# Optimization experiments

Measured on AMD Instinct MI355X. Metric: run time of the kernel, lower is better.

The kernel has to match this reference:

```python
import jax, jax.numpy as jnp
import numpy as np

HEAD_SIZE = 64

def setup_inputs() -> dict:
    key = jax.random.key(0)
    kx, kq, kk, kv = jax.random.split(key, 4)
    n_embd = 1024
    x = jax.random.normal(kx, (4, 2048, n_embd), dtype=jnp.float32)
    s = 1.0 / np.sqrt(n_embd)
    Wq = jax.random.normal(kq, (HEAD_SIZE, n_embd), dtype=jnp.float32) * s
    Wk = jax.random.normal(kk, (HEAD_SIZE, n_embd), dtype=jnp.float32) * s
    Wv = jax.random.normal(kv, (HEAD_SIZE, n_embd), dtype=jnp.float32) * s
    return {"x": x, "Wq": Wq, "Wk": Wk, "Wv": Wv}

def reference(x, Wq, Wk, Wv):
    # x: [B, T, C]; W*: [head_size, C] (torch nn.Linear weight layout, y = x @ W.T)
    B, T, C = x.shape
    q = jnp.einsum('btc,hc->bth', x, Wq)  # [B, T, H]
    k = jnp.einsum('btc,hc->bth', x, Wk)
    v = jnp.einsum('btc,hc->bth', x, Wv)
    att = jnp.einsum('bqh,bkh->bqk', q, k) / jnp.sqrt(jnp.float32(HEAD_SIZE))
    causal = jnp.tril(jnp.ones((T, T), dtype=bool))  # [T, T]
    att = jnp.where(causal, att, -jnp.inf)
    att = jax.nn.softmax(att, axis=-1)
    out = jnp.einsum('bqk,bkh->bqh', att, v)  # [B, T, H]
    return out
```

## Files before the change

### kernel.cpp

```cpp
#include <hip/hip_runtime.h>
#include <hip/hip_bf16.h>

#define NB 4
#define TT 2048
#define CC 1024
#define HS 64
#define L2E 1.4426950408889634f

typedef __attribute__((ext_vector_type(8))) short short8;
typedef __attribute__((ext_vector_type(4))) short short4v;
typedef __attribute__((ext_vector_type(4))) float floatx4;
typedef __attribute__((ext_vector_type(2))) float floatx2;

__device__ __forceinline__ short f2bf(float f) {
  union { float f; unsigned u; } x; x.f = f;
  unsigned r = (x.u + 0x7fffu + ((x.u >> 16) & 1u)) >> 16;
  return (short)r;
}

__device__ __forceinline__ short8 pack_bf16x8(floatx4 a, floatx4 b) {
  union { __hip_bfloat162 h[4]; short8 s; } u;
  u.h[0] = __float22bfloat162_rn(make_float2(a[0], a[1]));
  u.h[1] = __float22bfloat162_rn(make_float2(a[2], a[3]));
  u.h[2] = __float22bfloat162_rn(make_float2(b[0], b[1]));
  u.h[3] = __float22bfloat162_rn(make_float2(b[2], b[3]));
  return u.s;
}

#define KC 64
#define WTS 72

__global__ __launch_bounds__(768) void qkv_proj(const float* __restrict__ x,
                                                const float* __restrict__ wq,
                                                const float* __restrict__ wk,
                                                const float* __restrict__ wv,
                                                short* __restrict__ qb,
                                                short* __restrict__ kbuf,
                                                short* __restrict__ vtb) {
  __shared__ __align__(16) short wt[2][192 * WTS];
  __shared__ __align__(16) short xs[2][32 * WTS];

  const int tid  = threadIdx.x;
  const int lane = tid & 63;
  const int w    = tid >> 6;
  const int col  = lane & 15;
  const int quad = lane >> 4;
  const int row32 = blockIdx.x * 32;
  const int rg = w / 6;
  const int cg = w % 6;
  const int mat   = cg >> 1;
  const int hbase = (cg & 1) * 32;

  const int o0 = tid >> 3,         kk0 = (tid & 7) * 8;
  const int o1 = (768 + tid) >> 3, kk1 = ((768 + tid) & 7) * 8;
  const float* wsrc0 = (o0 < 64 ? wq + (size_t)o0 * CC
                                : wk + (size_t)(o0 - 64) * CC) + kk0;
  const float* wsrc1 = (o1 < 128 ? wk + (size_t)(o1 - 64) * CC
                                 : wv + (size_t)(o1 - 128) * CC) + kk1;
  const int xr = tid >> 3, xk = (tid & 7) * 8;
  const float* xsrc = x + (size_t)(row32 + xr) * CC + xk;

  floatx4 wa0 = *(const floatx4*)(wsrc0);
  floatx4 wc0 = *(const floatx4*)(wsrc0 + 4);
  floatx4 wa1 = *(const floatx4*)(wsrc1);
  floatx4 wc1 = *(const floatx4*)(wsrc1 + 4);
  floatx4 xA[2], xC[2];
  if (tid < 256) {
    xA[0] = *(const floatx4*)(xsrc);       xC[0] = *(const floatx4*)(xsrc + 4);
    xA[1] = *(const floatx4*)(xsrc + KC);  xC[1] = *(const floatx4*)(xsrc + KC + 4);
  }

  *(short8*)(&wt[0][o0 * WTS + kk0]) = pack_bf16x8(wa0, wc0);
  *(short8*)(&wt[0][o1 * WTS + kk1]) = pack_bf16x8(wa1, wc1);
  if (tid < 256) *(short8*)(&xs[0][xr * WTS + xk]) = pack_bf16x8(xA[0], xC[0]);
  __syncthreads();

  floatx4 acc0 = (floatx4){0.f, 0.f, 0.f, 0.f};
  floatx4 acc1 = (floatx4){0.f, 0.f, 0.f, 0.f};
  const int arow  = (rg * 16 + col) * WTS + quad * 8;
  const int brow0 = (cg * 32 + col) * WTS + quad * 8;
  const int brow1 = (cg * 32 + 16 + col) * WTS + quad * 8;

#pragma unroll 2
  for (int ch = 0; ch < 16; ++ch) {
    const int cur = ch & 1;
    if (ch < 15) {
      const int k0 = (ch + 1) * KC;
      wa0 = *(const floatx4*)(wsrc0 + k0);
      wc0 = *(const floatx4*)(wsrc0 + k0 + 4);
      wa1 = *(const floatx4*)(wsrc1 + k0);
      wc1 = *(const floatx4*)(wsrc1 + k0 + 4);
    }
    if (ch < 14 && tid < 256) {
      const int k0 = (ch + 2) * KC;
      xA[cur] = *(const floatx4*)(xsrc + k0);
      xC[cur] = *(const floatx4*)(xsrc + k0 + 4);
    }
#pragma unroll
    for (int kb2 = 0; kb2 < 2; ++kb2) {
      short8 a  = *(const short8*)(&xs[cur][arow + kb2 * 32]);
      short8 b0 = *(const short8*)(&wt[cur][brow0 + kb2 * 32]);
      short8 b1 = *(const short8*)(&wt[cur][brow1 + kb2 * 32]);
      acc0 = __builtin_amdgcn_mfma_f32_16x16x32_bf16(a, b0, acc0, 0, 0, 0);
      acc1 = __builtin_amdgcn_mfma_f32_16x16x32_bf16(a, b1, acc1, 0, 0, 0);
    }
    if (ch < 15) {
      __syncthreads();
      const int nxt = cur ^ 1;
      *(short8*)(&wt[nxt][o0 * WTS + kk0]) = pack_bf16x8(wa0, wc0);
      *(short8*)(&wt[nxt][o1 * WTS + kk1]) = pack_bf16x8(wa1, wc1);
      if (tid < 256)
        *(short8*)(&xs[nxt][xr * WTS + xk]) = pack_bf16x8(xA[nxt & 1], xC[nxt & 1]);
      __syncthreads();
    }
  }

  const int h0 = hbase + col;
  const int h1 = hbase + 16 + col;
  if (mat == 2) {
    int b = row32 >> 11;
    int t = (row32 & (TT - 1)) + rg * 16 + quad * 4;
    short4v o;
    o[0] = f2bf(acc0[0]); o[1] = f2bf(acc0[1]); o[2] = f2bf(acc0[2]); o[3] = f2bf(acc0[3]);
    *(short4v*)(vtb + (size_t)(b * HS + h0) * TT + t) = o;
    o[0] = f2bf(acc1[0]); o[1] = f2bf(acc1[1]); o[2] = f2bf(acc1[2]); o[3] = f2bf(acc1[3]);
    *(short4v*)(vtb + (size_t)(b * HS + h1) * TT + t) = o;
  } else {
    short* dst = (mat == 0) ? qb : kbuf;
    float s = (mat == 0) ? 0.125f : 1.0f;
#pragma unroll
    for (int r = 0; r < 4; ++r) {
      size_t row = (size_t)(row32 + rg * 16 + quad * 4 + r);
      dst[row * HS + h0] = f2bf(acc0[r] * s);
      dst[row * HS + h1] = f2bf(acc1[r] * s);
    }
  }
}

#define PST 72

__global__ __launch_bounds__(512, 4) void attn(const short* __restrict__ qb,
                                               const short* __restrict__ kb,
                                               const short* __restrict__ vtb,
                                               float* __restrict__ out) {
  __shared__ __align__(16) short pt[8][2][16 * PST];
  __shared__ float cl[8][16];
  __shared__ __align__(16) float co[8][16][64];

  const int tid  = threadIdx.x;
  const int lane = tid & 63;
  const int w    = tid >> 6;
  const int col  = lane & 15;
  const int quad = lane >> 4;
  const int b  = blockIdx.x & 3;
  const int qt = 127 - (blockIdx.x >> 2);
  const int t0 = qt * 16;

  const short* qbase = qb + (size_t)(b * TT + t0) * HS;
  const short* kbase = kb + (size_t)b * TT * HS;
  const short* vbase = vtb + (size_t)b * HS * TT;

  short8 qf0 = *(const short8*)(qbase + col * HS + quad * 8);
  short8 qf1 = *(const short8*)(qbase + col * HS + 32 + quad * 8);

  floatx4 oacc[4];
#pragma unroll
  for (int i = 0; i < 4; ++i) oacc[i] = (floatx4){0.f, 0.f, 0.f, 0.f};
  float lsum[4] = {0.f, 0.f, 0.f, 0.f};

  const int Nc = (t0 + 16 + 63) >> 6;

  short8 knA[4], knB[4];
  if (w < Nc) {
    const short* kp = kbase + (size_t)(w * 64) * HS + quad * 8;
#pragma unroll
    for (int j = 0; j < 4; ++j) {
      knA[j] = *(const short8*)(kp + (size_t)(j * 16 + col) * HS);
      knB[j] = *(const short8*)(kp + (size_t)(j * 16 + col) * HS + 32);
    }
  }

  int parity = 0;
  for (int c = w; c < Nc; c += 8, parity ^= 1) {
    const int kb0 = c * 64;

    floatx4 st[4];
#pragma unroll
    for (int j = 0; j < 4; ++j) st[j] = (floatx4){0.f, 0.f, 0.f, 0.f};
#pragma unroll
    for (int j = 0; j < 4; ++j) {
      st[j] = __builtin_amdgcn_mfma_f32_16x16x32_bf16(qf0, knA[j], st[j], 0, 0, 0);
      st[j] = __builtin_amdgcn_mfma_f32_16x16x32_bf16(qf1, knB[j], st[j], 0, 0, 0);
    }

    short8 vfA[4], vfB[4];
#pragma unroll
    for (int ht = 0; ht < 4; ++ht) {
      const short* vp = vbase + (size_t)(ht * 16 + col) * TT + kb0 + quad * 8;
      vfA[ht] = *(const short8*)(vp);
      vfB[ht] = *(const short8*)(vp + 32);
    }

    if (c + 8 < Nc) {
      const short* kpn = kbase + (size_t)((c + 8) * 64) * HS + quad * 8;
#pragma unroll
      for (int j = 0; j < 4; ++j) {
        knA[j] = *(const short8*)(kpn + (size_t)(j * 16 + col) * HS);
        knB[j] = *(const short8*)(kpn + (size_t)(j * 16 + col) * HS + 32);
      }
    }

    const bool diag = (kb0 + 63 > t0);
    short* pw = &pt[w][parity][0];

#pragma unroll
    for (int j = 0; j < 4; ++j) {
      if (diag) {
        int kcol = kb0 + j * 16 + col;
#pragma unroll
        for (int r = 0; r < 4; ++r)
          if (kcol > t0 + quad * 4 + r) st[j][r] = -1e30f;
      }
      float p0 = exp2f(st[j][0] * L2E);
      float p1 = exp2f(st[j][1] * L2E);
      float p2 = exp2f(st[j][2] * L2E);
      float p3 = exp2f(st[j][3] * L2E);
      lsum[0] += p0; lsum[1] += p1; lsum[2] += p2; lsum[3] += p3;
      union { __hip_bfloat162 h; short s[2]; } uA, uB;
      uA.h = __float22bfloat162_rn(make_float2(p0, p1));
      uB.h = __float22bfloat162_rn(make_float2(p2, p3));
      pw[(quad * 4 + 0) * PST + j * 16 + col] = uA.s[0];
      pw[(quad * 4 + 1) * PST + j * 16 + col] = uA.s[1];
      pw[(quad * 4 + 2) * PST + j * 16 + col] = uB.s[0];
      pw[(quad * 4 + 3) * PST + j * 16 + col] = uB.s[1];
    }
    short8 af0 = *(const short8*)(pw + col * PST + quad * 8);
    short8 af1 = *(const short8*)(pw + col * PST + 32 + quad * 8);

#pragma unroll
    for (int ht = 0; ht < 4; ++ht) {
      oacc[ht] = __builtin_amdgcn_mfma_f32_16x16x32_bf16(af0, vfA[ht], oacc[ht], 0, 0, 0);
      oacc[ht] = __builtin_amdgcn_mfma_f32_16x16x32_bf16(af1, vfB[ht], oacc[ht], 0, 0, 0);
    }
  }

#pragma unroll
  for (int r = 0; r < 4; ++r) {
#pragma unroll
    for (int off = 8; off; off >>= 1) lsum[r] += __shfl_xor(lsum[r], off);
    if (col == 0) cl[w][quad * 4 + r] = lsum[r];
#pragma unroll
    for (int ht = 0; ht < 4; ++ht)
      co[w][quad * 4 + r][ht * 16 + col] = oacc[ht][r];
  }
  __syncthreads();

  const int crow = tid >> 5;
  const int ch   = (tid & 31) << 1;
  float L = 0.f;
  floatx2 a = (floatx2){0.f, 0.f};
#pragma unroll
  for (int w2 = 0; w2 < 8; ++w2) {
    L += cl[w2][crow];
    floatx2 ov = *(const floatx2*)&co[w2][crow][ch];
    a[0] += ov[0]; a[1] += ov[1];
  }
  float inv = 1.0f / L;
  floatx2 res = (floatx2){a[0] * inv, a[1] * inv};
  *(floatx2*)(out + (size_t)(b * TT + t0 + crow) * HS + ch) = res;
}

extern "C" void kernel_launch(void* const* d_in, const int* in_sizes, int n_in,
                              void* d_out, int out_size, void* d_ws, size_t ws_size,
                              hipStream_t stream) {
  const float* x  = (const float*)d_in[0];
  const float* wq = (const float*)d_in[1];
  const float* wk = (const float*)d_in[2];
  const float* wv = (const float*)d_in[3];
  float* out = (float*)d_out;

  char* ws = (char*)d_ws;
  short* qbf = (short*)ws;
  short* kbf = (short*)(ws + 1048576);
  short* vtb = (short*)(ws + 2097152);

  hipLaunchKernelGGL(qkv_proj, dim3(256), dim3(768), 0, stream,
                     x, wq, wk, wv, qbf, kbf, vtb);
  hipLaunchKernelGGL(attn, dim3(512), dim3(512), 0, stream, qbf, kbf, vtb, out);
}
```

Baseline: 119.5 us.

## Deepen weight prefetch, transpose QK^T MFMA for vectorized P stores, add setprio

The projection kernel's weight loads are now double-buffered two chunks ahead, matching the existing x prefetch, so global latency has more time to hide. In the attention kernel the QK^T MFMA operands are swapped, so each lane holds four consecutive keys for one query. This lets the probabilities be written to LDS as one 4-wide store instead of four scalar stores, and the row sum is now reduced across quads rather than within columns. It also moves the next-K prefetch after the softmax and wraps the MFMA blocks in s_setprio, at the cost of more live registers.

```diff
diff --git a/kernel.cpp b/kernel.cpp
--- a/kernel.cpp
+++ b/kernel.cpp
@@ -60,18 +60,19 @@
   const int xr = tid >> 3, xk = (tid & 7) * 8;
   const float* xsrc = x + (size_t)(row32 + xr) * CC + xk;
 
-  floatx4 wa0 = *(const floatx4*)(wsrc0);
-  floatx4 wc0 = *(const floatx4*)(wsrc0 + 4);
-  floatx4 wa1 = *(const floatx4*)(wsrc1);
-  floatx4 wc1 = *(const floatx4*)(wsrc1 + 4);
+  floatx4 wA0[2], wC0[2], wA1[2], wC1[2];
+  wA0[0] = *(const floatx4*)(wsrc0);       wC0[0] = *(const floatx4*)(wsrc0 + 4);
+  wA1[0] = *(const floatx4*)(wsrc1);       wC1[0] = *(const floatx4*)(wsrc1 + 4);
+  wA0[1] = *(const floatx4*)(wsrc0 + KC);  wC0[1] = *(const floatx4*)(wsrc0 + KC + 4);
+  wA1[1] = *(const floatx4*)(wsrc1 + KC);  wC1[1] = *(const floatx4*)(wsrc1 + KC + 4);
   floatx4 xA[2], xC[2];
   if (tid < 256) {
     xA[0] = *(const floatx4*)(xsrc);       xC[0] = *(const floatx4*)(xsrc + 4);
     xA[1] = *(const floatx4*)(xsrc + KC);  xC[1] = *(const floatx4*)(xsrc + KC + 4);
   }
 
-  *(short8*)(&wt[0][o0 * WTS + kk0]) = pack_bf16x8(wa0, wc0);
-  *(short8*)(&wt[0][o1 * WTS + kk1]) = pack_bf16x8(wa1, wc1);
+  *(short8*)(&wt[0][o0 * WTS + kk0]) = pack_bf16x8(wA0[0], wC0[0]);
+  *(short8*)(&wt[0][o1 * WTS + kk1]) = pack_bf16x8(wA1[0], wC1[0]);
   if (tid < 256) *(short8*)(&xs[0][xr * WTS + xk]) = pack_bf16x8(xA[0], xC[0]);
   __syncthreads();
 
@@ -84,12 +85,12 @@
 #pragma unroll 2
   for (int ch = 0; ch < 16; ++ch) {
     const int cur = ch & 1;
-    if (ch < 15) {
-      const int k0 = (ch + 1) * KC;
-      wa0 = *(const floatx4*)(wsrc0 + k0);
-      wc0 = *(const floatx4*)(wsrc0 + k0 + 4);
-      wa1 = *(const floatx4*)(wsrc1 + k0);
-      wc1 = *(const floatx4*)(wsrc1 + k0 + 4);
+    if (ch < 14) {
+      const int k0 = (ch + 2) * KC;
+      wA0[cur] = *(const floatx4*)(wsrc0 + k0);
+      wC0[cur] = *(const floatx4*)(wsrc0 + k0 + 4);
+      wA1[cur] = *(const floatx4*)(wsrc1 + k0);
+      wC1[cur] = *(const floatx4*)(wsrc1 + k0 + 4);
     }
     if (ch < 14 && tid < 256) {
       const int k0 = (ch + 2) * KC;
@@ -107,10 +108,10 @@
     if (ch < 15) {
       __syncthreads();
       const int nxt = cur ^ 1;
-      *(short8*)(&wt[nxt][o0 * WTS + kk0]) = pack_bf16x8(wa0, wc0);
-      *(short8*)(&wt[nxt][o1 * WTS + kk1]) = pack_bf16x8(wa1, wc1);
+      *(short8*)(&wt[nxt][o0 * WTS + kk0]) = pack_bf16x8(wA0[nxt], wC0[nxt]);
+      *(short8*)(&wt[nxt][o1 * WTS + kk1]) = pack_bf16x8(wA1[nxt], wC1[nxt]);
       if (tid < 256)
-        *(short8*)(&xs[nxt][xr * WTS + xk]) = pack_bf16x8(xA[nxt & 1], xC[nxt & 1]);
+        *(short8*)(&xs[nxt][xr * WTS + xk]) = pack_bf16x8(xA[nxt], xC[nxt]);
       __syncthreads();
     }
   }
@@ -166,7 +167,7 @@
   floatx4 oacc[4];
 #pragma unroll
   for (int i = 0; i < 4; ++i) oacc[i] = (floatx4){0.f, 0.f, 0.f, 0.f};
-  float lsum[4] = {0.f, 0.f, 0.f, 0.f};
+  float lsum = 0.f;
 
   const int Nc = (t0 + 16 + 63) >> 6;
 
@@ -187,11 +188,13 @@
     floatx4 st[4];
 #pragma unroll
     for (int j = 0; j < 4; ++j) st[j] = (floatx4){0.f, 0.f, 0.f, 0.f};
+    __builtin_amdgcn_s_setprio(1);
 #pragma unroll
     for (int j = 0; j < 4; ++j) {
-      st[j] = __builtin_amdgcn_mfma_f32_16x16x32_bf16(qf0, knA[j], st[j], 0, 0, 0);
-      st[j] = __builtin_amdgcn_mfma_f32_16x16x32_bf16(qf1, knB[j], st[j], 0, 0, 0);
-    }
+      st[j] = __builtin_amdgcn_mfma_f32_16x16x32_bf16(knA[j], qf0, st[j], 0, 0, 0);
+      st[j] = __builtin_amdgcn_mfma_f32_16x16x32_bf16(knB[j], qf1, st[j], 0, 0, 0);
+    }
+    __builtin_amdgcn_s_setprio(0);
 
     short8 vfA[4], vfB[4];
 #pragma unroll
@@ -201,58 +204,60 @@
       vfB[ht] = *(const short8*)(vp + 32);
     }
 
-    if (c + 8 < Nc) {
-      const short* kpn = kbase + (size_t)((c + 8) * 64) * HS + quad * 8;
-#pragma unroll
-      for (int j = 0; j < 4; ++j) {
-        knA[j] = *(const short8*)(kpn + (size_t)(j * 16 + col) * HS);
-        knB[j] = *(const short8*)(kpn + (size_t)(j * 16 + col) * HS + 32);
-      }
-    }
-
     const bool diag = (kb0 + 63 > t0);
     short* pw = &pt[w][parity][0];
+    const int qi = t0 + col;
 
 #pragma unroll
     for (int j = 0; j < 4; ++j) {
       if (diag) {
-        int kcol = kb0 + j * 16 + col;
+        int kidx = kb0 + j * 16 + quad * 4;
 #pragma unroll
         for (int r = 0; r < 4; ++r)
-          if (kcol > t0 + quad * 4 + r) st[j][r] = -1e30f;
+          if (kidx + r > qi) st[j][r] = -1e30f;
       }
       float p0 = exp2f(st[j][0] * L2E);
       float p1 = exp2f(st[j][1] * L2E);
       float p2 = exp2f(st[j][2] * L2E);
       float p3 = exp2f(st[j][3] * L2E);
-      lsum[0] += p0; lsum[1] += p1; lsum[2] += p2; lsum[3] += p3;
+      lsum += (p0 + p1) + (p2 + p3);
       union { __hip_bfloat162 h; short s[2]; } uA, uB;
       uA.h = __float22bfloat162_rn(make_float2(p0, p1));
       uB.h = __float22bfloat162_rn(make_float2(p2, p3));
-      pw[(quad * 4 + 0) * PST + j * 16 + col] = uA.s[0];
-      pw[(quad * 4 + 1) * PST + j * 16 + col] = uA.s[1];
-      pw[(quad * 4 + 2) * PST + j * 16 + col] = uB.s[0];
-      pw[(quad * 4 + 3) * PST + j * 16 + col] = uB.s[1];
-    }
+      short4v o4;
+      o4[0] = uA.s[0]; o4[1] = uA.s[1]; o4[2] = uB.s[0]; o4[3] = uB.s[1];
+      *(short4v*)(pw + col * PST + j * 16 + quad * 4) = o4;
+    }
+
+    if (c + 8 < Nc) {
+      const short* kpn = kbase + (size_t)((c + 8) * 64) * HS + quad * 8;
+#pragma unroll
+      for (int j = 0; j < 4; ++j) {
+        knA[j] = *(const short8*)(kpn + (size_t)(j * 16 + col) * HS);
+        knB[j] = *(const short8*)(kpn + (size_t)(j * 16 + col) * HS + 32);
+      }
+    }
+
     short8 af0 = *(const short8*)(pw + col * PST + quad * 8);
     short8 af1 = *(const short8*)(pw + col * PST + 32 + quad * 8);
 
+    __builtin_amdgcn_s_setprio(1);
 #pragma unroll
     for (int ht = 0; ht < 4; ++ht) {
       oacc[ht] = __builtin_amdgcn_mfma_f32_16x16x32_bf16(af0, vfA[ht], oacc[ht], 0, 0, 0);
       oacc[ht] = __builtin_amdgcn_mfma_f32_16x16x32_bf16(af1, vfB[ht], oacc[ht], 0, 0, 0);
     }
-  }
-
-#pragma unroll
-  for (int r = 0; r < 4; ++r) {
-#pragma unroll
-    for (int off = 8; off; off >>= 1) lsum[r] += __shfl_xor(lsum[r], off);
-    if (col == 0) cl[w][quad * 4 + r] = lsum[r];
+    __builtin_amdgcn_s_setprio(0);
+  }
+
+  lsum += __shfl_xor(lsum, 16);
+  lsum += __shfl_xor(lsum, 32);
+  if (lane < 16) cl[w][lane] = lsum;
+#pragma unroll
+  for (int r = 0; r < 4; ++r)
 #pragma unroll
     for (int ht = 0; ht < 4; ++ht)
       co[w][quad * 4 + r][ht * 16 + col] = oacc[ht][r];
-  }
   __syncthreads();
 
   const int crow = tid >> 5;
```

New measurement: 112.3 us. 6.0% less time.
